# Optimization experiments

Hardware: AMD Instinct MI355X
Metric: run time of the kernel (lower is better)

Reference implementation:

```python
import jax, jax.numpy as jnp
import numpy as np
from jax import lax

N = 19
ACT_DIM = 12
_SRC = np.array([0,1,2,3,4,5,6,7,8,9,10,11,12,13,14,15,16,17,18,1,2,3,4,5,6,7,8,9,10,11,12,13,14,15,16,17], dtype=np.int64)
_DST = np.array([1,2,3,4,5,6,7,8,9,10,11,12,13,14,15,16,17,18,17,0,1,2,3,4,5,6,7,8,9,10,11,12,13,14,15,16], dtype=np.int64)
SRC = jnp.asarray(_SRC)
DST = jnp.asarray(_DST)
# GAT/GCN in PyG add self-loops by default
SRC_SL = jnp.concatenate([SRC, jnp.arange(N)])
DST_SL = jnp.concatenate([DST, jnp.arange(N)])


def _lin(v, W, b=None):
    y = v @ W.T
    return y + b if b is not None else y


def _minmax(v):
    return (v - v.min()) / (v.max() - v.min())


def _conv(x, w, b, pad):
    y = lax.conv_general_dilated(x, w, (2, 2), [(pad, pad), (pad, pad)], dimension_numbers=('NCHW', 'OIHW', 'NCHW'))
    return y + b[None, :, None, None]


def _sage_layer(h, lw, lb, rw):
    # SAGEConv(aggr='add'): lin_l(sum_{j->i} x_j) + lin_r(x_i); lin_r has no bias
    agg = jax.ops.segment_sum(h[SRC], DST, num_segments=N)
    return agg @ lw.T + lb + h @ rw.T


def _gat(h, W, a_s, a_d, b):
    # GATConv heads=1, leaky_relu slope 0.2, softmax over incoming edges (incl. self-loop)
    hh = h @ W.T
    es, ed = hh @ a_s, hh @ a_d
    e = jax.nn.leaky_relu(es[SRC_SL] + ed[DST_SL], 0.2)
    m = jax.ops.segment_max(e, DST_SL, num_segments=N)
    ex = jnp.exp(e - m[DST_SL])
    den = jax.ops.segment_sum(ex, DST_SL, num_segments=N)
    alpha = ex / den[DST_SL]
    return jax.ops.segment_sum(alpha[:, None] * hh[SRC_SL], DST_SL, num_segments=N) + b


def _gcn(h, W, b):
    # GCNConv(improved=True): A_hat = A + 2I, D^{-1/2} A_hat D^{-1/2}
    hh = h @ W.T
    w_e = jnp.concatenate([jnp.ones(SRC.shape[0], jnp.float32), 2.0 * jnp.ones(N, jnp.float32)])
    deg = jax.ops.segment_sum(w_e, DST_SL, num_segments=N)
    dinv = lax.rsqrt(deg)
    norm = dinv[SRC_SL] * dinv[DST_SL] * w_e
    return jax.ops.segment_sum(norm[:, None] * hh[SRC_SL], DST_SL, num_segments=N) + b


def setup_inputs() -> dict:
    ks = iter(jax.random.split(jax.random.key(0), 64))
    def nrm(*shape):
        return jax.random.normal(next(ks), shape, jnp.float32) * 0.02
    d = dict(
        x=jax.random.normal(next(ks), (1, 128, 128), jnp.float32),
        state=jax.random.normal(next(ks), (20,), jnp.float32),
        x_graph=jax.random.normal(next(ks), (19,), jnp.float32),
        c1w=nrm(32, 1, 5, 5), c1b=nrm(32),
        c2w=nrm(32, 32, 5, 5), c2b=nrm(32),
        c3w=nrm(32, 32, 5, 5), c3b=nrm(32),
        fc0w=nrm(6000, 6272), fc0b=nrm(6000),
        fc1w=nrm(100, 6000), fc1b=nrm(100),
        fc2w=nrm(100, 20), fc2b=nrm(100),
        fc3w=nrm(100, 100), fc3b=nrm(100),
        sg1a_lw=nrm(1000, 1), sg1a_lb=nrm(1000), sg1a_rw=nrm(1000, 1),
        sg1b_lw=nrm(1000, 1000), sg1b_lb=nrm(1000), sg1b_rw=nrm(1000, 1000),
        gat2_w=nrm(1000, 1000), gat2_as=nrm(1000), gat2_ad=nrm(1000), gat2_b=nrm(1000),
        sg3a_lw=nrm(1000, 1000), sg3a_lb=nrm(1000), sg3a_rw=nrm(1000, 1000),
        sg3b_lw=nrm(1000, 1000), sg3b_lb=nrm(1000), sg3b_rw=nrm(1000, 1000),
        gat4_w=nrm(1000, 1000), gat4_as=nrm(1000), gat4_ad=nrm(1000), gat4_b=nrm(1000),
        gcn_w=nrm(1000, 1000), gcn_b=nrm(1000),
        fcg_w=nrm(100, 1000), fcg_b=nrm(100),
        fc4w=nrm(200, 300), fc4b=nrm(200),
        mu_w=nrm(ACT_DIM, 200), mu_b=nrm(ACT_DIM),
        log_sigma=jnp.zeros((ACT_DIM,), jnp.float32),
        cr_w=nrm(1, 200), cr_b=nrm(1),
    )
    return d


def reference(x, state, x_graph, c1w, c1b, c2w, c2b, c3w, c3b, fc0w, fc0b, fc1w, fc1b, fc2w, fc2b, fc3w, fc3b, sg1a_lw, sg1a_lb, sg1a_rw, sg1b_lw, sg1b_lb, sg1b_rw, gat2_w, gat2_as, gat2_ad, gat2_b, sg3a_lw, sg3a_lb, sg3a_rw, sg3b_lw, sg3b_lb, sg3b_rw, gat4_w, gat4_as, gat4_ad, gat4_b, gcn_w, gcn_b, fcg_w, fcg_b, fc4w, fc4b, mu_w, mu_b, log_sigma, cr_w, cr_b):
    relu = jax.nn.relu
    xc = x[None]                       # [1,1,128,128]
    xc = relu(_conv(xc, c1w, c1b, 1))  # [1,32,63,63]
    xc = relu(_conv(xc, c2w, c2b, 0))  # [1,32,30,30]
    xc = _conv(xc, c3w, c3b, 1)        # [1,32,14,14] (no relu after conv3 in source)
    v = xc.reshape(-1)                 # 6272
    v = _lin(_lin(v, fc0w, fc0b), fc1w, fc1b)
    n1 = _minmax(v)
    s = _lin(_lin(state, fc2w, fc2b), fc3w, fc3b)
    n2 = _minmax(s)
    h = x_graph[:, None]               # [19,1]
    h = relu(_sage_layer(h, sg1a_lw, sg1a_lb, sg1a_rw))   # GraphSAGE layer 1 (inner ReLU)
    h = relu(_sage_layer(h, sg1b_lw, sg1b_lb, sg1b_rw))   # layer 2, then outer ReLU (idempotent)
    h = relu(_gat(h, gat2_w, gat2_as, gat2_ad, gat2_b))
    h = relu(_sage_layer(h, sg3a_lw, sg3a_lb, sg3a_rw))
    h = relu(_sage_layer(h, sg3b_lw, sg3b_lb, sg3b_rw))
    h = relu(_gat(h, gat4_w, gat4_as, gat4_ad, gat4_b))
    h = _gcn(h, gcn_w, gcn_b)
    g = _lin(h.mean(0), fcg_w, fcg_b)
    n3 = _minmax(g)
    feats = _lin(jnp.concatenate([n1, n2, n3]), fc4w, fc4b)
    mu = jnp.tanh(_lin(feats, mu_w, mu_b))
    sigma = jnp.exp(log_sigma)
    value = _lin(feats, cr_w, cr_b)
    return (mu, sigma, value)
```

## Files before the change

kernel.cpp:

```cpp
#include <hip/hip_runtime.h>
#include <math.h>

#define DEV __device__ __forceinline__

constexpr int ESRC[36] = {0,1,2,3,4,5,6,7,8,9,10,11,12,13,14,15,16,17,18,1,2,3,4,5,6,7,8,9,10,11,12,13,14,15,16,17};
constexpr int EDST[36] = {1,2,3,4,5,6,7,8,9,10,11,12,13,14,15,16,17,18,17,0,1,2,3,4,5,6,7,8,9,10,11,12,13,14,15,16};
constexpr int SSRC[55] = {0,1,2,3,4,5,6,7,8,9,10,11,12,13,14,15,16,17,18,1,2,3,4,5,6,7,8,9,10,11,12,13,14,15,16,17,
                          0,1,2,3,4,5,6,7,8,9,10,11,12,13,14,15,16,17,18};
constexpr int SDST[55] = {1,2,3,4,5,6,7,8,9,10,11,12,13,14,15,16,17,18,17,0,1,2,3,4,5,6,7,8,9,10,11,12,13,14,15,16,
                          0,1,2,3,4,5,6,7,8,9,10,11,12,13,14,15,16,17,18};
constexpr float DINV[19] = {0.5773502691896258f,0.5f,0.5f,0.5f,0.5f,0.5f,0.5f,0.5f,0.5f,0.5f,
                            0.5f,0.5f,0.5f,0.5f,0.5f,0.5f,0.5f,0.5f,0.5773502691896258f};

constexpr int WS_C1  = 0;
constexpr int WS_C2  = 127008;
constexpr int WS_V   = 155808;
constexpr int WS_FC0 = 162080;
constexpr int WS_N1  = 168080;
constexpr int WS_N2  = 168180;
constexpr int WS_FC0B= 206280;
constexpr int WS_PB  = 264384;
constexpr int WS_PC  = 340384;
constexpr int WS_FC0C= 416384;
constexpr int WS_FC0D= 422384;
constexpr int WS_PH2 = 428384;
constexpr int WS_N3  = 504384;
constexpr int WS_FEAT= 504584;

DEV float wredsum(float v){
  #pragma unroll
  for (int o = 32; o; o >>= 1) v += __shfl_xor(v, o);
  return v;
}
DEV float d4(float4 a, float4 b){ return a.x*b.x + a.y*b.y + a.z*b.z + a.w*b.w; }

DEV void sage_split2(int blk, int tid, float* sm,
                     const float* pin, const float* pbias,
                     const float* lw, const float* rw, float* pout)
{
  const int cg_ = blk >> 2, kq = blk & 3;
  const int kb = kq*256;
  const int cntf = (kq < 3) ? 256 : 232;
  const int cnt4 = cntf >> 2;
  float* hS = sm;
  float* aS = sm + 19*256;
  for (int c = tid; c < 19*256; c += 256){
    const int n = c >> 8, j = c & 255;
    if (j < cntf){
      const int i = kb + j;
      const float v = pin[n*1000+i] + pin[(19+n)*1000+i] + pin[(38+n)*1000+i]
                    + pin[(57+n)*1000+i] + pbias[i];
      hS[c] = fmaxf(v, 0.f);
    }
  }
  __syncthreads();
  if (tid < cntf){
    float hv[19];
    #pragma unroll
    for (int n=0;n<19;++n) hv[n] = hS[n*256 + tid];
    float ag[19];
    #pragma unroll
    for (int n=0;n<19;++n) ag[n] = 0.f;
    #pragma unroll
    for (int e=0;e<36;++e) ag[EDST[e]] += hv[ESRC[e]];
    #pragma unroll
    for (int n=0;n<19;++n) aS[n*256 + tid] = ag[n];
  }
  __syncthreads();
  const int lane = tid & 63, wv = tid >> 6;
  const int i0 = cg_*8 + 2*wv, i1 = i0 + 1;
  float acc0[19], acc1[19];
  #pragma unroll
  for (int n=0;n<19;++n){ acc0[n]=0.f; acc1[n]=0.f; }
  if (lane < cnt4){
    const float4 wl0 = *((const float4*)(lw + i0*1000) + kq*64 + lane);
    const float4 wl1 = *((const float4*)(lw + i1*1000) + kq*64 + lane);
    const float4 wr0 = *((const float4*)(rw + i0*1000) + kq*64 + lane);
    const float4 wr1 = *((const float4*)(rw + i1*1000) + kq*64 + lane);
    const float4* h4 = (const float4*)hS;
    const float4* a4 = (const float4*)aS;
    #pragma unroll
    for (int n=0;n<19;++n){
      const float4 hv = h4[n*64+lane], av = a4[n*64+lane];
      acc0[n] = d4(wl0,av) + d4(wr0,hv);
      acc1[n] = d4(wl1,av) + d4(wr1,hv);
    }
  }
  #pragma unroll
  for (int n=0;n<19;++n){ acc0[n]=wredsum(acc0[n]); acc1[n]=wredsum(acc1[n]); }
  if (lane == 0){
    #pragma unroll
    for (int n=0;n<19;++n){
      pout[(kq*19+n)*1000 + i0] = acc0[n];
      pout[(kq*19+n)*1000 + i1] = acc1[n];
    }
  }
}

DEV void sage1b_fused(int blk, int tid, float* sm, const float* xg,
                      const float* alw, const float* alb, const float* arw,
                      const float* lw, const float* rw, float* pout)
{
  const int cg_ = blk >> 2, kq = blk & 3;
  const int kb = kq*256;
  const int cntf = (kq < 3) ? 256 : 232;
  const int cnt4 = cntf >> 2;
  float* hS = sm;
  float* aS = sm + 19*256;
  float xv[19];
  #pragma unroll
  for (int n=0;n<19;++n) xv[n] = xg[n];
  float ag0[19];
  #pragma unroll
  for (int n=0;n<19;++n) ag0[n] = 0.f;
  #pragma unroll
  for (int e=0;e<36;++e) ag0[EDST[e]] += xv[ESRC[e]];
  if (tid < cntf){
    const int i = kb + tid;
    const float a = alw[i], bb = alb[i], r = arw[i];
    float hv[19];
    #pragma unroll
    for (int n=0;n<19;++n){ hv[n] = fmaxf(a*ag0[n] + bb + r*xv[n], 0.f); hS[n*256+tid] = hv[n]; }
    float ag[19];
    #pragma unroll
    for (int n=0;n<19;++n) ag[n] = 0.f;
    #pragma unroll
    for (int e=0;e<36;++e) ag[EDST[e]] += hv[ESRC[e]];
    #pragma unroll
    for (int n=0;n<19;++n) aS[n*256+tid] = ag[n];
  }
  __syncthreads();
  const int lane = tid & 63, wv = tid >> 6;
  const int i0 = cg_*8 + 2*wv, i1 = i0 + 1;
  float acc0[19], acc1[19];
  #pragma unroll
  for (int n=0;n<19;++n){ acc0[n]=0.f; acc1[n]=0.f; }
  if (lane < cnt4){
    const float4 wl0 = *((const float4*)(lw + i0*1000) + kq*64 + lane);
    const float4 wl1 = *((const float4*)(lw + i1*1000) + kq*64 + lane);
    const float4 wr0 = *((const float4*)(rw + i0*1000) + kq*64 + lane);
    const float4 wr1 = *((const float4*)(rw + i1*1000) + kq*64 + lane);
    const float4* h4 = (const float4*)hS;
    const float4* a4 = (const float4*)aS;
    #pragma unroll
    for (int n=0;n<19;++n){
      const float4 hv = h4[n*64+lane], av = a4[n*64+lane];
      acc0[n] = d4(wl0,av) + d4(wr0,hv);
      acc1[n] = d4(wl1,av) + d4(wr1,hv);
    }
  }
  #pragma unroll
  for (int n=0;n<19;++n){ acc0[n]=wredsum(acc0[n]); acc1[n]=wredsum(acc1[n]); }
  if (lane == 0){
    #pragma unroll
    for (int n=0;n<19;++n){
      pout[(kq*19+n)*1000 + i0] = acc0[n];
      pout[(kq*19+n)*1000 + i1] = acc1[n];
    }
  }
}

DEV void gatmat_split2(int blk, int tid, float* sm,
                       const float* pin, const float* pbias,
                       const float* W, float* pout)
{
  const int cg_ = blk >> 2, kq = blk & 3;
  const int kb = kq*256;
  const int cntf = (kq < 3) ? 256 : 232;
  const int cnt4 = cntf >> 2;
  float* hS = sm;
  for (int c = tid; c < 19*256; c += 256){
    const int n = c >> 8, j = c & 255;
    if (j < cntf){
      const int i = kb + j;
      const float v = pin[n*1000+i] + pin[(19+n)*1000+i] + pin[(38+n)*1000+i]
                    + pin[(57+n)*1000+i] + pbias[i];
      hS[c] = fmaxf(v, 0.f);
    }
  }
  __syncthreads();
  const int lane = tid & 63, wv = tid >> 6;
  const int i0 = cg_*8 + 2*wv, i1 = i0 + 1;
  float acc0[19], acc1[19];
  #pragma unroll
  for (int n=0;n<19;++n){ acc0[n]=0.f; acc1[n]=0.f; }
  if (lane < cnt4){
    const float4 w0 = *((const float4*)(W + i0*1000) + kq*64 + lane);
    const float4 w1 = *((const float4*)(W + i1*1000) + kq*64 + lane);
    const float4* h4 = (const float4*)hS;
    #pragma unroll
    for (int n=0;n<19;++n){
      const float4 hv = h4[n*64+lane];
      acc0[n] = d4(w0,hv);
      acc1[n] = d4(w1,hv);
    }
  }
  #pragma unroll
  for (int n=0;n<19;++n){ acc0[n]=wredsum(acc0[n]); acc1[n]=wredsum(acc1[n]); }
  if (lane == 0){
    #pragma unroll
    for (int n=0;n<19;++n){
      pout[(kq*19+n)*1000 + i0] = acc0[n];
      pout[(kq*19+n)*1000 + i1] = acc1[n];
    }
  }
}

DEV void alpha_sm(int t, float* sm, const float* ph, const float* as_,
                  const float* ad_)
{
  const int lane = t & 63, wv = t >> 6;
  float es[19], ed[19];
  #pragma unroll
  for (int n=0;n<19;++n){ es[n]=0.f; ed[n]=0.f; }
  for (int k = t; k < 1000; k += 256){
    const float asv = as_[k], adv = ad_[k];
    #pragma unroll
    for (int n=0;n<19;++n){
      const float hh = ph[n*1000+k] + ph[(19+n)*1000+k] + ph[(38+n)*1000+k] + ph[(57+n)*1000+k];
      es[n] += hh*asv; ed[n] += hh*adv;
    }
  }
  #pragma unroll
  for (int n=0;n<19;++n){ es[n]=wredsum(es[n]); ed[n]=wredsum(ed[n]); }
  if (lane == 0){
    #pragma unroll
    for (int n=0;n<19;++n){ sm[wv*38+n]=es[n]; sm[wv*38+19+n]=ed[n]; }
  }
  __syncthreads();
  if (t < 38) sm[152+t] = sm[t] + sm[38+t] + sm[76+t] + sm[114+t];
  __syncthreads();
  if (t < 55){
    float e = sm[152+SSRC[t]] + sm[171+SDST[t]];
    sm[200+t] = e > 0.f ? e : 0.2f*e;
  }
  __syncthreads();
  if (t < 19){
    float m = -1e30f;
    #pragma unroll
    for (int e=0;e<55;++e) if (SDST[e]==t) m = fmaxf(m, sm[200+e]);
    float den = 0.f;
    #pragma unroll
    for (int e=0;e<55;++e) if (SDST[e]==t) den += expf(sm[200+e]-m);
    sm[260+t]=m; sm[280+t]=den;
  }
  __syncthreads();
  if (t < 55) sm[320+t] = expf(sm[200+t]-sm[260+SDST[t]]) / sm[280+SDST[t]];
  __syncthreads();
}

DEV void sage3a_fused(int blk, int t, float* sm, const float* ph,
                      const float* as_, const float* ad_, const float* bias,
                      const float* lw, const float* rw, float* pout)
{
  alpha_sm(t, sm, ph, as_, ad_);
  const int cg_ = blk >> 2, kq = blk & 3;
  const int kb = kq*256;
  const int cntf = (kq < 3) ? 256 : 232;
  const int cnt4 = cntf >> 2;
  float* hS = sm + 384;
  float* aS = sm + 384 + 4864;
  if (t < cntf){
    const int i = kb + t;
    float hin[19];
    #pragma unroll
    for (int n=0;n<19;++n)
      hin[n] = ph[n*1000+i] + ph[(19+n)*1000+i] + ph[(38+n)*1000+i] + ph[(57+n)*1000+i];
    float acc[19];
    #pragma unroll
    for (int n=0;n<19;++n) acc[n]=0.f;
    #pragma unroll
    for (int e=0;e<55;++e) acc[SDST[e]] += sm[320+e]*hin[SSRC[e]];
    const float bi = bias[i];
    float hv[19];
    #pragma unroll
    for (int n=0;n<19;++n){ hv[n] = fmaxf(acc[n]+bi, 0.f); hS[n*256+t] = hv[n]; }
    float ag[19];
    #pragma unroll
    for (int n=0;n<19;++n) ag[n]=0.f;
    #pragma unroll
    for (int e=0;e<36;++e) ag[EDST[e]] += hv[ESRC[e]];
    #pragma unroll
    for (int n=0;n<19;++n) aS[n*256+t] = ag[n];
  }
  __syncthreads();
  const int lane = t & 63, wv = t >> 6;
  const int i0 = cg_*8 + 2*wv, i1 = i0 + 1;
  float acc0[19], acc1[19];
  #pragma unroll
  for (int n=0;n<19;++n){ acc0[n]=0.f; acc1[n]=0.f; }
  if (lane < cnt4){
    const float4 wl0 = *((const float4*)(lw + i0*1000) + kq*64 + lane);
    const float4 wl1 = *((const float4*)(lw + i1*1000) + kq*64 + lane);
    const float4 wr0 = *((const float4*)(rw + i0*1000) + kq*64 + lane);
    const float4 wr1 = *((const float4*)(rw + i1*1000) + kq*64 + lane);
    const float4* h4 = (const float4*)hS;
    const float4* a4 = (const float4*)aS;
    #pragma unroll
    for (int n=0;n<19;++n){
      const float4 hv = h4[n*64+lane], av = a4[n*64+lane];
      acc0[n] = d4(wl0,av) + d4(wr0,hv);
      acc1[n] = d4(wl1,av) + d4(wr1,hv);
    }
  }
  #pragma unroll
  for (int n=0;n<19;++n){ acc0[n]=wredsum(acc0[n]); acc1[n]=wredsum(acc1[n]); }
  if (lane == 0){
    #pragma unroll
    for (int n=0;n<19;++n){
      pout[(kq*19+n)*1000 + i0] = acc0[n];
      pout[(kq*19+n)*1000 + i1] = acc1[n];
    }
  }
}

DEV void gcn_fused_task(int blk, int t, float* sm, const float* ph,
                        const float* as_, const float* ad_, const float* bias,
                        const float* W, float* pout)
{
  alpha_sm(t, sm, ph, as_, ad_);
  const int cg_ = blk >> 2, kq = blk & 3;
  const int kb = kq*256;
  const int cntf = (kq < 3) ? 256 : 232;
  const int cnt4 = cntf >> 2;
  float* hS = sm + 384;
  if (t < cntf){
    const int i = kb + t;
    float hv[19];
    #pragma unroll
    for (int n=0;n<19;++n)
      hv[n] = ph[n*1000+i] + ph[(19+n)*1000+i] + ph[(38+n)*1000+i] + ph[(57+n)*1000+i];
    float acc[19];
    #pragma unroll
    for (int n=0;n<19;++n) acc[n]=0.f;
    #pragma unroll
    for (int e=0;e<55;++e) acc[SDST[e]] += sm[320+e]*hv[SSRC[e]];
    const float bi = bias[i];
    #pragma unroll
    for (int n=0;n<19;++n) hS[n*256+t] = fmaxf(acc[n]+bi, 0.f);
  }
  __syncthreads();
  const int lane = t & 63, wv = t >> 6;
  const int i0 = cg_*8 + 2*wv, i1 = i0 + 1;
  float acc0[19], acc1[19];
  #pragma unroll
  for (int n=0;n<19;++n){ acc0[n]=0.f; acc1[n]=0.f; }
  if (lane < cnt4){
    const float4 w0 = *((const float4*)(W + i0*1000) + kq*64 + lane);
    const float4 w1 = *((const float4*)(W + i1*1000) + kq*64 + lane);
    const float4* h4 = (const float4*)hS;
    #pragma unroll
    for (int n=0;n<19;++n){
      const float4 hv = h4[n*64+lane];
      acc0[n] = d4(w0,hv);
      acc1[n] = d4(w1,hv);
    }
  }
  #pragma unroll
  for (int n=0;n<19;++n){ acc0[n]=wredsum(acc0[n]); acc1[n]=wredsum(acc1[n]); }
  if (lane == 0){
    #pragma unroll
    for (int n=0;n<19;++n){
      pout[(kq*19+n)*1000 + i0] = acc0[n];
      pout[(kq*19+n)*1000 + i1] = acc1[n];
    }
  }
}

DEV void conv1_task(int task, int t, const float* x, const float* c1w,
                    const float* c1b, float* ws)
{
  const int idx = task*256 + t;
  if (idx < 127008){
    const int oc = idx/3969, r = idx - oc*3969, oy = r/63, ox = r - oy*63;
    const float* wp = c1w + oc*25;
    float acc = c1b[oc];
    #pragma unroll
    for (int ky=0;ky<5;++ky){
      const int iy = oy*2 - 1 + ky;
      if ((unsigned)iy < 128u){
        #pragma unroll
        for (int kx=0;kx<5;++kx){
          const int ix = ox*2 - 1 + kx;
          if ((unsigned)ix < 128u) acc += x[iy*128+ix]*wp[ky*5+kx];
        }
      }
    }
    ws[WS_C1+idx] = fmaxf(acc, 0.f);
  }
}

DEV void conv2_task(int task, int t, float* sm, const float* c2w,
                    const float* c2b, float* ws)
{
  const int oc = task >> 2, q = task & 3;
  const int r0 = q*16;
  const int nout = (q < 3) ? 240 : 180;
  float* buf0 = sm; float* buf1 = sm + 4788;
  float rv[19];
  #pragma unroll
  for (int u=0; u<19; ++u){
    const int c = t + u*256; float v = 0.f;
    if (c < 4788){
      const int p = c/1197, r = c - p*1197, lr = r/63, xx = r - lr*63;
      const int iy = r0 + lr;
      if (iy < 63) v = ws[WS_C1 + p*3969 + iy*63 + xx];
    }
    rv[u] = v;
  }
  #pragma unroll
  for (int u=0; u<19; ++u){ const int c = t+u*256; if (c<4788) buf0[c]=rv[u]; }
  __syncthreads();
  const int oy_l = t/30, ox = t - oy_l*30;
  float acc = (t < nout) ? c2b[oc] : 0.f;
  for (int g=0; g<8; ++g){
    float* cur = (g&1) ? buf1 : buf0;
    if (g < 7){
      #pragma unroll
      for (int u=0; u<19; ++u){
        const int c = t + u*256; float v = 0.f;
        if (c < 4788){
          const int p = c/1197, r = c - p*1197, lr = r/63, xx = r - lr*63;
          const int iy = r0 + lr;
          if (iy < 63) v = ws[WS_C1 + (4*(g+1)+p)*3969 + iy*63 + xx];
        }
        rv[u] = v;
      }
    }
    if (t < nout){
      #pragma unroll
      for (int p=0;p<4;++p){
        const float* wp = c2w + (oc*32 + 4*g + p)*25;
        const float* ip = cur + p*1197 + (2*oy_l)*63 + 2*ox;
        #pragma unroll
        for (int ky=0;ky<5;++ky)
          #pragma unroll
          for (int kx=0;kx<5;++kx)
            acc += ip[ky*63+kx]*wp[ky*5+kx];
      }
    }
    if (g < 7){
      __syncthreads();
      float* nxt = (g&1) ? buf0 : buf1;
      #pragma unroll
      for (int u=0; u<19; ++u){ const int c = t+u*256; if (c<4788) nxt[c]=rv[u]; }
      __syncthreads();
    }
  }
  if (t < nout){
    const int oy = q*8 + oy_l;
    ws[WS_C2 + oc*900 + oy*30 + ox] = fmaxf(acc, 0.f);
  }
}

DEV void conv3_task(int oc, int t, float* sm, const float* c3w,
                    const float* c3b, float* ws)
{
  float* buf0 = sm; float* buf1 = sm + 3600;
  float rv[15];
  #pragma unroll
  for (int u=0; u<15; ++u){
    const int c = t + u*256;
    rv[u] = (c < 3600) ? ws[WS_C2 + c] : 0.f;
  }
  #pragma unroll
  for (int u=0; u<15; ++u){ const int c = t+u*256; if (c<3600) buf0[c]=rv[u]; }
  __syncthreads();
  const int oy = t/14, ox = t - oy*14;
  float acc = (t < 196) ? c3b[oc] : 0.f;
  for (int g=0; g<8; ++g){
    float* cur = (g&1) ? buf1 : buf0;
    if (g < 7){
      #pragma unroll
      for (int u=0; u<15; ++u){
        const int c = t + u*256;
        rv[u] = (c < 3600) ? ws[WS_C2 + (g+1)*3600 + c] : 0.f;
      }
    }
    if (t < 196){
      #pragma unroll
      for (int p=0;p<4;++p){
        const float* wp = c3w + (oc*32 + 4*g + p)*25;
        const float* ip = cur + p*900;
        #pragma unroll
        for (int ky=0;ky<5;++ky){
          const int iy = oy*2 - 1 + ky;
          if ((unsigned)iy < 30u){
            #pragma unroll
            for (int kx=0;kx<5;++kx){
              const int ix = ox*2 - 1 + kx;
              if ((unsigned)ix < 30u) acc += ip[iy*30+ix]*wp[ky*5+kx];
            }
          }
        }
      }
    }
    if (g < 7){
      __syncthreads();
      float* nxt = (g&1) ? buf0 : buf1;
      #pragma unroll
      for (int u=0; u<15; ++u){ const int c = t+u*256; if (c<3600) nxt[c]=rv[u]; }
      __syncthreads();
    }
  }
  if (t < 196) ws[WS_V + oc*196 + t] = acc;
}

DEV void fc0_task(int task, int t, const float* fc0w, float* ws)
{
  const int lane = t & 63, wv = t >> 6;
  const int rq = task >> 2, q = task & 3;
  const int row = rq*4 + wv;
  const float4* vr = (const float4*)(ws + WS_V) + q*392;
  const float4* wr = (const float4*)(fc0w) + (size_t)row*1568 + q*392;
  float4 wreg[6];
  #pragma unroll
  for (int u=0; u<6; ++u) wreg[u] = wr[u*64 + lane];
  float4 wtail;
  if (lane < 8) wtail = wr[384 + lane];
  float acc = 0.f;
  #pragma unroll
  for (int u=0; u<6; ++u) acc += d4(wreg[u], vr[u*64 + lane]);
  if (lane < 8) acc += d4(wtail, vr[384 + lane]);
  acc = wredsum(acc);
  if (lane == 0){
    float* pout = ws + (q==0 ? WS_FC0 : q==1 ? WS_FC0B : q==2 ? WS_FC0C : WS_FC0D);
    pout[row] = acc;
  }
}

__global__ __launch_bounds__(256) void k_ac_1(
    const float* __restrict__ x, const float* __restrict__ c1w, const float* __restrict__ c1b,
    const float* __restrict__ xg,
    const float* __restrict__ s1alw, const float* __restrict__ s1alb, const float* __restrict__ s1arw,
    const float* __restrict__ s1blw, const float* __restrict__ s1brw,
    const float* __restrict__ stt, const float* __restrict__ fc2w, const float* __restrict__ fc2b,
    const float* __restrict__ fc3w, const float* __restrict__ fc3b,
    float* __restrict__ ws)
{
  __shared__ __align__(16) float sm[9728];
  const int b = blockIdx.x, t = threadIdx.x;
  if (b < 497){
    conv1_task(b, t, x, c1w, c1b, ws);
  } else if (b < 997){
    sage1b_fused(b-497, t, sm, xg, s1alw, s1alb, s1arw, s1blw, s1brw, ws+WS_PB);
  } else {
    if (t < 100){
      float acc = fc2b[t];
      #pragma unroll
      for (int k=0;k<20;++k) acc += fc2w[t*20+k]*stt[k];
      sm[t] = acc;
    }
    __syncthreads();
    if (t < 100){
      float acc = fc3b[t];
      for (int k=0;k<100;++k) acc += fc3w[t*100+k]*sm[k];
      ws[WS_N2+t] = acc;
    }
  }
}

__global__ __launch_bounds__(256) void k_ac_2(
    const float* __restrict__ c2w, const float* __restrict__ c2b,
    const float* __restrict__ s1blb, const float* __restrict__ g2w,
    float* __restrict__ ws)
{
  __shared__ __align__(16) float sm[9728];
  const int b = blockIdx.x, t = threadIdx.x;
  if (b < 128) conv2_task(b, t, sm, c2w, c2b, ws);
  else gatmat_split2(b-128, t, sm, ws+WS_PB, s1blb, g2w, ws+WS_PH2);
}

__global__ __launch_bounds__(256) void k_ac_3(
    const float* __restrict__ c3w, const float* __restrict__ c3b,
    const float* __restrict__ g2as, const float* __restrict__ g2ad, const float* __restrict__ g2b,
    const float* __restrict__ s3alw, const float* __restrict__ s3arw,
    float* __restrict__ ws)
{
  __shared__ __align__(16) float sm[10112];
  const int b = blockIdx.x, t = threadIdx.x;
  if (b < 32) conv3_task(b, t, sm, c3w, c3b, ws);
  else sage3a_fused(b-32, t, sm, ws+WS_PH2, g2as, g2ad, g2b, s3alw, s3arw, ws+WS_PB);
}

__global__ __launch_bounds__(256) void k_ac_4(
    const float* __restrict__ fc0w,
    const float* __restrict__ s3alb, const float* __restrict__ s3blw, const float* __restrict__ s3brw,
    float* __restrict__ ws)
{
  __shared__ __align__(16) float sm[9728];
  const int b = blockIdx.x, t = threadIdx.x;
  if (b < 6000) fc0_task(b, t, fc0w, ws);
  else sage_split2(b-6000, t, sm, ws+WS_PB, s3alb, s3blw, s3brw, ws+WS_PC);
}

__global__ __launch_bounds__(256) void k_ac_5(
    const float* __restrict__ fc1w, const float* __restrict__ fc1b,
    const float* __restrict__ fc0b,
    const float* __restrict__ s3blb, const float* __restrict__ g4w,
    float* __restrict__ ws)
{
  __shared__ __align__(16) float sm[4864];
  const int b = blockIdx.x, t = threadIdx.x;
  if (b < 100){
    const int row = b, lane = t & 63, wv = t >> 6;
    const float4* wr = (const float4*)(fc1w + row*6000);
    const float4* p0 = (const float4*)(ws + WS_FC0);
    const float4* p1 = (const float4*)(ws + WS_FC0B);
    const float4* p2 = (const float4*)(ws + WS_FC0C);
    const float4* p3 = (const float4*)(ws + WS_FC0D);
    const float4* bb = (const float4*)fc0b;
    float acc = 0.f;
    #pragma unroll
    for (int u=0; u<6; ++u){
      const int j = t + u*256;
      if (j < 1500){
        const float4 a0=p0[j], a1=p1[j], a2=p2[j], a3=p3[j], bv=bb[j];
        const float4 s = make_float4(a0.x+a1.x+a2.x+a3.x+bv.x, a0.y+a1.y+a2.y+a3.y+bv.y,
                                     a0.z+a1.z+a2.z+a3.z+bv.z, a0.w+a1.w+a2.w+a3.w+bv.w);
        acc += d4(wr[j], s);
      }
    }
    acc = wredsum(acc);
    if (lane == 0) sm[wv] = acc;
    __syncthreads();
    if (t == 0) ws[WS_N1+row] = sm[0]+sm[1]+sm[2]+sm[3] + fc1b[row];
  } else {
    gatmat_split2(b-100, t, sm, ws+WS_PC, s3blb, g4w, ws+WS_PH2);
  }
}

__global__ __launch_bounds__(256) void k_ac_6(
    const float* __restrict__ g4as, const float* __restrict__ g4ad, const float* __restrict__ g4b,
    const float* __restrict__ gcnw, float* __restrict__ ws)
{
  __shared__ __align__(16) float sm[5248];
  gcn_fused_task(blockIdx.x, threadIdx.x, sm, ws+WS_PH2, g4as, g4ad, g4b, gcnw, ws+WS_PB);
}

__global__ __launch_bounds__(256) void k_ac_7(
    const float* __restrict__ gcnb, const float* __restrict__ fcgw, const float* __restrict__ fcgb,
    float* __restrict__ ws)
{
  __shared__ float sm[4];
  const int b = blockIdx.x, t = threadIdx.x, lane = t & 63, wv = t >> 6;
  float cc[19];
  #pragma unroll
  for (int m=0;m<19;++m) cc[m] = 2.f*DINV[m]*DINV[m];
  #pragma unroll
  for (int e=0;e<36;++e) cc[ESRC[e]] += DINV[ESRC[e]]*DINV[EDST[e]];
  #pragma unroll
  for (int m=0;m<19;++m) cc[m] *= (1.f/19.f);
  const float* pb = ws + WS_PB;
  const float* wrow = fcgw + b*1000;
  float acc = 0.f;
  #pragma unroll
  for (int u=0; u<4; ++u){
    const int i = t + u*256;
    if (i < 1000){
      float gv = gcnb[i];
      #pragma unroll
      for (int m=0;m<19;++m){
        const float hh = pb[m*1000+i] + pb[(19+m)*1000+i] + pb[(38+m)*1000+i] + pb[(57+m)*1000+i];
        gv += cc[m]*hh;
      }
      acc += wrow[i]*gv;
    }
  }
  acc = wredsum(acc);
  if (lane == 0) sm[wv] = acc;
  __syncthreads();
  if (t == 0) ws[WS_N3+b] = sm[0]+sm[1]+sm[2]+sm[3] + fcgb[b];
}

__global__ __launch_bounds__(256) void k_ac_8(
    const float* __restrict__ fc4w, const float* __restrict__ fc4b,
    float* __restrict__ ws)
{
  __shared__ __align__(16) float f[300];
  __shared__ float mnmx[6];
  const int b = blockIdx.x, t = threadIdx.x, lane = t & 63, wv = t >> 6;
  for (int c = t; c < 300; c += 256){
    f[c] = (c < 100) ? ws[WS_N1 + c]
         : (c < 200) ? ws[WS_N2 + c - 100]
                     : ws[WS_N3 + c - 200];
  }
  __syncthreads();
  if (wv < 3){
    const int base = wv*100;
    const float v  = f[base + lane];
    const float v2 = (lane < 36) ? f[base + 64 + lane] : v;
    float mn = fminf(v, v2), mx = fmaxf(v, v2);
    #pragma unroll
    for (int o=32;o;o>>=1){ mn = fminf(mn, __shfl_xor(mn,o)); mx = fmaxf(mx, __shfl_xor(mx,o)); }
    if (lane == 0){ mnmx[wv*2]=mn; mnmx[wv*2+1]=mx; }
  }
  __syncthreads();
  for (int c = t; c < 300; c += 256){
    const int g = c/100;
    f[c] = (f[c]-mnmx[g*2])/(mnmx[g*2+1]-mnmx[g*2]);
  }
  __syncthreads();
  const int row = b*4 + wv;
  const float* wp = fc4w + row*300;
  float acc = 0.f;
  #pragma unroll
  for (int it=0; it<5; ++it){
    const int k = it*64 + lane;
    if (k < 300) acc += wp[k]*f[k];
  }
  acc = wredsum(acc);
  if (lane == 0) ws[WS_FEAT+row] = acc + fc4b[row];
}

__global__ __launch_bounds__(256) void k_ac_9(
    const float* __restrict__ muw, const float* __restrict__ mub,
    const float* __restrict__ lsig, const float* __restrict__ crw, const float* __restrict__ crb,
    float* __restrict__ ws, float* __restrict__ out)
{
  __shared__ __align__(16) float feats[200];
  const int t = threadIdx.x, lane = t & 63, wv = t >> 6;
  if (t < 200) feats[t] = ws[WS_FEAT + t];
  if (t >= 200 && t < 212) out[t - 188] = expf(lsig[t-200]);
  __syncthreads();
  #pragma unroll
  for (int rr=0; rr<4; ++rr){
    const int row = wv + rr*4;
    if (row < 12){
      const float* wp = muw + row*200;
      float a = 0.f;
      #pragma unroll
      for (int it=0; it<4; ++it){
        const int k = it*64 + lane;
        if (k < 200) a += wp[k]*feats[k];
      }
      a = wredsum(a);
      if (lane == 0) out[row] = tanhf(a + mub[row]);
    } else if (row == 12){
      float a = 0.f;
      #pragma unroll
      for (int it=0; it<4; ++it){
        const int k = it*64 + lane;
        if (k < 200) a += crw[k]*feats[k];
      }
      a = wredsum(a);
      if (lane == 0) out[24] = a + crb[0];
    }
  }
}

extern "C" void kernel_launch(void* const* d_in, const int* in_sizes, int n_in,
                              void* d_out, int out_size, void* d_ws, size_t ws_size,
                              hipStream_t stream)
{
  (void)in_sizes; (void)n_in; (void)out_size; (void)ws_size;
  const float* x     = (const float*)d_in[0];
  const float* stt   = (const float*)d_in[1];
  const float* xg    = (const float*)d_in[2];
  const float* c1w   = (const float*)d_in[3];
  const float* c1b   = (const float*)d_in[4];
  const float* c2w   = (const float*)d_in[5];
  const float* c2b   = (const float*)d_in[6];
  const float* c3w   = (const float*)d_in[7];
  const float* c3b   = (const float*)d_in[8];
  const float* fc0w  = (const float*)d_in[9];
  const float* fc0b  = (const float*)d_in[10];
  const float* fc1w  = (const float*)d_in[11];
  const float* fc1b  = (const float*)d_in[12];
  const float* fc2w  = (const float*)d_in[13];
  const float* fc2b  = (const float*)d_in[14];
  const float* fc3w  = (const float*)d_in[15];
  const float* fc3b  = (const float*)d_in[16];
  const float* s1alw = (const float*)d_in[17];
  const float* s1alb = (const float*)d_in[18];
  const float* s1arw = (const float*)d_in[19];
  const float* s1blw = (const float*)d_in[20];
  const float* s1blb = (const float*)d_in[21];
  const float* s1brw = (const float*)d_in[22];
  const float* g2w   = (const float*)d_in[23];
  const float* g2as  = (const float*)d_in[24];
  const float* g2ad  = (const float*)d_in[25];
  const float* g2b   = (const float*)d_in[26];
  const float* s3alw = (const float*)d_in[27];
  const float* s3alb = (const float*)d_in[28];
  const float* s3arw = (const float*)d_in[29];
  const float* s3blw = (const float*)d_in[30];
  const float* s3blb = (const float*)d_in[31];
  const float* s3brw = (const float*)d_in[32];
  const float* g4w   = (const float*)d_in[33];
  const float* g4as  = (const float*)d_in[34];
  const float* g4ad  = (const float*)d_in[35];
  const float* g4b   = (const float*)d_in[36];
  const float* gcnw  = (const float*)d_in[37];
  const float* gcnb  = (const float*)d_in[38];
  const float* fcgw  = (const float*)d_in[39];
  const float* fcgb  = (const float*)d_in[40];
  const float* fc4w  = (const float*)d_in[41];
  const float* fc4b  = (const float*)d_in[42];
  const float* muw   = (const float*)d_in[43];
  const float* mub   = (const float*)d_in[44];
  const float* lsig  = (const float*)d_in[45];
  const float* crw   = (const float*)d_in[46];
  const float* crb   = (const float*)d_in[47];
  float* ws  = (float*)d_ws;
  float* out = (float*)d_out;

  k_ac_1 <<<dim3(998),  dim3(256), 0, stream>>>(x, c1w, c1b, xg, s1alw, s1alb, s1arw,
                                                s1blw, s1brw, stt, fc2w, fc2b, fc3w, fc3b, ws);
  k_ac_2 <<<dim3(628),  dim3(256), 0, stream>>>(c2w, c2b, s1blb, g2w, ws);
  k_ac_3 <<<dim3(532),  dim3(256), 0, stream>>>(c3w, c3b, g2as, g2ad, g2b, s3alw, s3arw, ws);
  k_ac_4 <<<dim3(6500), dim3(256), 0, stream>>>(fc0w, s3alb, s3blw, s3brw, ws);
  k_ac_5 <<<dim3(600),  dim3(256), 0, stream>>>(fc1w, fc1b, fc0b, s3blb, g4w, ws);
  k_ac_6 <<<dim3(500),  dim3(256), 0, stream>>>(g4as, g4ad, g4b, gcnw, ws);
  k_ac_7 <<<dim3(100),  dim3(256), 0, stream>>>(gcnb, fcgw, fcgb, ws);
  k_ac_8 <<<dim3(50),   dim3(256), 0, stream>>>(fc4w, fc4b, ws);
  k_ac_9 <<<dim3(1),    dim3(256), 0, stream>>>(muw, mub, lsig, crw, crb, ws, out);
}
```

Baseline: 290.8 us.

## Split fc0 into halves and reschedule sage/gat stages across kernels

The fc0 matvec now splits each row into two halves instead of four, so each wave loads twelve float4 registers plus a tail and there are half as many blocks and partial buffers. The sage3b stage moves out of the fc0 kernel and into the fc1 kernel, and the gat4 matmul gets its own new kernel. This gives a ten-kernel chain. The intent is a smaller fc0 kernel that no longer carries shared-memory-heavy sage blocks, at the cost of one more launch and higher register pressure per thread.

```diff
diff --git a/kernel.cpp b/kernel.cpp
--- a/kernel.cpp
+++ b/kernel.cpp
@@ -21,8 +21,6 @@
 constexpr int WS_FC0B= 206280;
 constexpr int WS_PB  = 264384;
 constexpr int WS_PC  = 340384;
-constexpr int WS_FC0C= 416384;
-constexpr int WS_FC0D= 422384;
 constexpr int WS_PH2 = 428384;
 constexpr int WS_N3  = 504384;
 constexpr int WS_FEAT= 504584;
@@ -506,29 +504,6 @@
   if (t < 196) ws[WS_V + oc*196 + t] = acc;
 }
 
-DEV void fc0_task(int task, int t, const float* fc0w, float* ws)
-{
-  const int lane = t & 63, wv = t >> 6;
-  const int rq = task >> 2, q = task & 3;
-  const int row = rq*4 + wv;
-  const float4* vr = (const float4*)(ws + WS_V) + q*392;
-  const float4* wr = (const float4*)(fc0w) + (size_t)row*1568 + q*392;
-  float4 wreg[6];
-  #pragma unroll
-  for (int u=0; u<6; ++u) wreg[u] = wr[u*64 + lane];
-  float4 wtail;
-  if (lane < 8) wtail = wr[384 + lane];
-  float acc = 0.f;
-  #pragma unroll
-  for (int u=0; u<6; ++u) acc += d4(wreg[u], vr[u*64 + lane]);
-  if (lane < 8) acc += d4(wtail, vr[384 + lane]);
-  acc = wredsum(acc);
-  if (lane == 0){
-    float* pout = ws + (q==0 ? WS_FC0 : q==1 ? WS_FC0B : q==2 ? WS_FC0C : WS_FC0D);
-    pout[row] = acc;
-  }
-}
-
 __global__ __launch_bounds__(256) void k_ac_1(
     const float* __restrict__ x, const float* __restrict__ c1w, const float* __restrict__ c1b,
     const float* __restrict__ xg,
@@ -584,40 +559,52 @@
 }
 
 __global__ __launch_bounds__(256) void k_ac_4(
-    const float* __restrict__ fc0w,
-    const float* __restrict__ s3alb, const float* __restrict__ s3blw, const float* __restrict__ s3brw,
-    float* __restrict__ ws)
-{
-  __shared__ __align__(16) float sm[9728];
+    const float* __restrict__ fc0w, float* __restrict__ ws)
+{
   const int b = blockIdx.x, t = threadIdx.x;
-  if (b < 6000) fc0_task(b, t, fc0w, ws);
-  else sage_split2(b-6000, t, sm, ws+WS_PB, s3alb, s3blw, s3brw, ws+WS_PC);
+  const int lane = t & 63, wv = t >> 6;
+  const int half = b & 1, rowq = b >> 1;
+  const int row = rowq*4 + wv;
+  const float4* vr = (const float4*)(ws + WS_V) + half*784;
+  const float4* wr = (const float4*)(fc0w) + (size_t)row*1568 + half*784;
+  float4 wreg[12];
+  #pragma unroll
+  for (int u=0; u<12; ++u) wreg[u] = wr[u*64 + lane];
+  float4 wtail;
+  if (lane < 16) wtail = wr[768 + lane];
+  float acc = 0.f;
+  #pragma unroll
+  for (int u=0; u<12; ++u) acc += d4(wreg[u], vr[u*64 + lane]);
+  if (lane < 16) acc += d4(wtail, vr[768 + lane]);
+  acc = wredsum(acc);
+  if (lane == 0){
+    float* pout = ws + (half ? WS_FC0B : WS_FC0);
+    pout[row] = acc;
+  }
 }
 
 __global__ __launch_bounds__(256) void k_ac_5(
     const float* __restrict__ fc1w, const float* __restrict__ fc1b,
     const float* __restrict__ fc0b,
-    const float* __restrict__ s3blb, const float* __restrict__ g4w,
+    const float* __restrict__ s3alb, const float* __restrict__ s3blw, const float* __restrict__ s3brw,
     float* __restrict__ ws)
 {
-  __shared__ __align__(16) float sm[4864];
+  __shared__ __align__(16) float sm[9728];
   const int b = blockIdx.x, t = threadIdx.x;
   if (b < 100){
     const int row = b, lane = t & 63, wv = t >> 6;
     const float4* wr = (const float4*)(fc1w + row*6000);
     const float4* p0 = (const float4*)(ws + WS_FC0);
     const float4* p1 = (const float4*)(ws + WS_FC0B);
-    const float4* p2 = (const float4*)(ws + WS_FC0C);
-    const float4* p3 = (const float4*)(ws + WS_FC0D);
     const float4* bb = (const float4*)fc0b;
     float acc = 0.f;
     #pragma unroll
     for (int u=0; u<6; ++u){
       const int j = t + u*256;
       if (j < 1500){
-        const float4 a0=p0[j], a1=p1[j], a2=p2[j], a3=p3[j], bv=bb[j];
-        const float4 s = make_float4(a0.x+a1.x+a2.x+a3.x+bv.x, a0.y+a1.y+a2.y+a3.y+bv.y,
-                                     a0.z+a1.z+a2.z+a3.z+bv.z, a0.w+a1.w+a2.w+a3.w+bv.w);
+        const float4 a0=p0[j], a1=p1[j], bv=bb[j];
+        const float4 s = make_float4(a0.x+a1.x+bv.x, a0.y+a1.y+bv.y,
+                                     a0.z+a1.z+bv.z, a0.w+a1.w+bv.w);
         acc += d4(wr[j], s);
       }
     }
@@ -626,11 +613,18 @@
     __syncthreads();
     if (t == 0) ws[WS_N1+row] = sm[0]+sm[1]+sm[2]+sm[3] + fc1b[row];
   } else {
-    gatmat_split2(b-100, t, sm, ws+WS_PC, s3blb, g4w, ws+WS_PH2);
+    sage_split2(b-100, t, sm, ws+WS_PB, s3alb, s3blw, s3brw, ws+WS_PC);
   }
 }
 
 __global__ __launch_bounds__(256) void k_ac_6(
+    const float* __restrict__ s3blb, const float* __restrict__ g4w, float* __restrict__ ws)
+{
+  __shared__ __align__(16) float sm[4864];
+  gatmat_split2(blockIdx.x, threadIdx.x, sm, ws+WS_PC, s3blb, g4w, ws+WS_PH2);
+}
+
+__global__ __launch_bounds__(256) void k_ac_7(
     const float* __restrict__ g4as, const float* __restrict__ g4ad, const float* __restrict__ g4b,
     const float* __restrict__ gcnw, float* __restrict__ ws)
 {
@@ -638,7 +632,7 @@
   gcn_fused_task(blockIdx.x, threadIdx.x, sm, ws+WS_PH2, g4as, g4ad, g4b, gcnw, ws+WS_PB);
 }
 
-__global__ __launch_bounds__(256) void k_ac_7(
+__global__ __launch_bounds__(256) void k_ac_8(
     const float* __restrict__ gcnb, const float* __restrict__ fcgw, const float* __restrict__ fcgb,
     float* __restrict__ ws)
 {
@@ -673,7 +667,7 @@
   if (t == 0) ws[WS_N3+b] = sm[0]+sm[1]+sm[2]+sm[3] + fcgb[b];
 }
 
-__global__ __launch_bounds__(256) void k_ac_8(
+__global__ __launch_bounds__(256) void k_ac_9(
     const float* __restrict__ fc4w, const float* __restrict__ fc4b,
     float* __restrict__ ws)
 {
@@ -713,7 +707,7 @@
   if (lane == 0) ws[WS_FEAT+row] = acc + fc4b[row];
 }
 
-__global__ __launch_bounds__(256) void k_ac_9(
+__global__ __launch_bounds__(256) void k_ac_10(
     const float* __restrict__ muw, const float* __restrict__ mub,
     const float* __restrict__ lsig, const float* __restrict__ crw, const float* __restrict__ crb,
     float* __restrict__ ws, float* __restrict__ out)
@@ -809,10 +803,11 @@
                                                 s1blw, s1brw, stt, fc2w, fc2b, fc3w, fc3b, ws);
   k_ac_2 <<<dim3(628),  dim3(256), 0, stream>>>(c2w, c2b, s1blb, g2w, ws);
   k_ac_3 <<<dim3(532),  dim3(256), 0, stream>>>(c3w, c3b, g2as, g2ad, g2b, s3alw, s3arw, ws);
-  k_ac_4 <<<dim3(6500), dim3(256), 0, stream>>>(fc0w, s3alb, s3blw, s3brw, ws);
-  k_ac_5 <<<dim3(600),  dim3(256), 0, stream>>>(fc1w, fc1b, fc0b, s3blb, g4w, ws);
-  k_ac_6 <<<dim3(500),  dim3(256), 0, stream>>>(g4as, g4ad, g4b, gcnw, ws);
-  k_ac_7 <<<dim3(100),  dim3(256), 0, stream>>>(gcnb, fcgw, fcgb, ws);
-  k_ac_8 <<<dim3(50),   dim3(256), 0, stream>>>(fc4w, fc4b, ws);
-  k_ac_9 <<<dim3(1),    dim3(256), 0, stream>>>(muw, mub, lsig, crw, crb, ws, out);
-}
+  k_ac_4 <<<dim3(3000), dim3(256), 0, stream>>>(fc0w, ws);
+  k_ac_5 <<<dim3(600),  dim3(256), 0, stream>>>(fc1w, fc1b, fc0b, s3alb, s3blw, s3brw, ws);
+  k_ac_6 <<<dim3(500),  dim3(256), 0, stream>>>(s3blb, g4w, ws);
+  k_ac_7 <<<dim3(500),  dim3(256), 0, stream>>>(g4as, g4ad, g4b, gcnw, ws);
+  k_ac_8 <<<dim3(100),  dim3(256), 0, stream>>>(gcnb, fcgw, fcgb, ws);
+  k_ac_9 <<<dim3(50),   dim3(256), 0, stream>>>(fc4w, fc4b, ws);
+  k_ac_10<<<dim3(1),    dim3(256), 0, stream>>>(muw, mub, lsig, crw, crb, ws, out);
+}
```

After: 294.0 us. No clear change (+1.1%).
